# Performance work log

Hardware: AMD Instinct MI355X
Metric: run time of the kernel (lower is better)

## Reference

```python
import jax, jax.numpy as jnp
import numpy as np

NUM_NODES = 100000
NUM_EDGES = 1600000
FEAT = 128
HID = 128
NUM_GRAPHS = 512


def setup_inputs() -> dict:
    key = jax.random.key(0)
    ks = jax.random.split(key, 8)
    x = jax.random.normal(ks[0], (NUM_NODES, FEAT), dtype=jnp.float32)
    edge_index = jax.random.randint(ks[1], (2, NUM_EDGES), 0, NUM_NODES, dtype=jnp.int64)
    batch = jnp.sort(jax.random.randint(ks[2], (NUM_NODES,), 0, NUM_GRAPHS, dtype=jnp.int64))
    # Glorot-ish init for weights (scale named for clarity)
    s1 = 1.0 / np.sqrt(FEAT)
    s2 = 1.0 / np.sqrt(HID)
    W1 = jax.random.normal(ks[3], (FEAT, HID), dtype=jnp.float32) * s1
    b1 = jnp.zeros((HID,), dtype=jnp.float32)
    W2 = jax.random.normal(ks[4], (HID, HID), dtype=jnp.float32) * s2
    b2 = jnp.zeros((HID,), dtype=jnp.float32)
    Wout = jax.random.normal(ks[5], (HID, 1), dtype=jnp.float32) * s2
    bout = jnp.zeros((1,), dtype=jnp.float32)
    return {"x": x, "edge_index": edge_index, "batch": batch,
            "W1": W1, "b1": b1, "W2": W2, "b2": b2, "Wout": Wout, "bout": bout}


def reference(x, edge_index, batch, W1, b1, W2, b2, Wout, bout):
    N = x.shape[0]
    # PyG GCNConv: add self-loops, symmetric normalization D^-1/2 (A+I) D^-1/2
    loops = jnp.arange(N, dtype=edge_index.dtype)
    src = jnp.concatenate([edge_index[0], loops])  # [E+N]
    dst = jnp.concatenate([edge_index[1], loops])  # [E+N]
    ones = jnp.ones_like(dst, dtype=x.dtype)
    deg = jax.ops.segment_sum(ones, dst, num_segments=N)  # in-degree incl. self-loop
    dinv = jnp.where(deg > 0, jax.lax.rsqrt(deg), 0.0)
    coeff = (dinv[src] * dinv[dst])[:, None]  # [E+N, 1]

    def gcn(h, W, b):
        h = h @ W                                       # [N, H] dense GEMM
        msg = h[src] * coeff                            # gather + scale
        agg = jax.ops.segment_sum(msg, dst, num_segments=N)  # scatter-add
        return agg + b

    h = jax.nn.relu(gcn(x, W1, b1))
    h = jax.nn.relu(gcn(h, W2, b2))

    # global_mean_pool over batch ids
    G = NUM_GRAPHS
    sums = jax.ops.segment_sum(h, batch, num_segments=G)
    cnts = jax.ops.segment_sum(jnp.ones((N,), dtype=h.dtype), batch, num_segments=G)
    pooled = sums / jnp.maximum(cnts, 1.0)[:, None]

    return pooled @ Wout + bout  # [G, 1]
```

## Files before the change

kernel.cpp:

```cpp
#include <hip/hip_runtime.h>
#include <hip/hip_bf16.h>
#include <hip/hip_fp16.h>

#define FEAT 128
#define PSLOTS 64
#define BCAP 5120
#define NBIN 1024
#define NDEG 1024

typedef _Float16 h8 __attribute__((ext_vector_type(8)));
typedef float f4 __attribute__((ext_vector_type(4)));
typedef float fx2 __attribute__((ext_vector_type(2)));


__device__ __forceinline__ void wt_body(const float* __restrict__ W1,
                                        const float* __restrict__ W2,
                                        __half* __restrict__ Wt1,
                                        __half* __restrict__ Wt2, int bid) {
    int t = bid * 256 + threadIdx.x;
    const float* W = (t < 8192) ? W1 : W2;
    __half* Wt     = (t < 8192) ? Wt1 : Wt2;
    int u = t & 8191;
    int n = u >> 6, k2 = (u & 63) * 2;
    float a = W[(size_t)k2 * 128 + n];
    float b = W[(size_t)(k2 + 1) * 128 + n];
    ((__half2*)Wt)[n * 64 + (k2 >> 1)] = __floats2half2_rn(a, b);
}


__global__ __launch_bounds__(256) void k_pre(const int* __restrict__ ei, int E, int chunk,
                                             int* __restrict__ deg,
                                             const float* __restrict__ W1,
                                             const float* __restrict__ W2,
                                             __half* __restrict__ Wt1,
                                             __half* __restrict__ Wt2,
                                             unsigned char* __restrict__ padrow) {
    int bid = blockIdx.x;
    if (bid < NDEG) {
        int start = bid * chunk;
        int end = start + chunk; if (end > E) end = E;
        for (int e = start + threadIdx.x; e < end; e += 256)
            atomicAdd(&deg[ei[E + e]], 1);
    } else if (bid < NDEG + 64) {
        wt_body(W1, W2, Wt1, Wt2, bid - NDEG);
    } else {
        if (threadIdx.x < 8) ((uint4*)padrow)[threadIdx.x] = make_uint4(0, 0, 0, 0);
    }
}

__device__ __forceinline__ void bin_body(const int* __restrict__ ei, int E, int chunk,
                                         int* __restrict__ cursor,
                                         unsigned* __restrict__ binned, int nb,
                                         int bid, int* smem) {
    int* hist = smem;
    int* base = smem + 512;
    int start = bid * chunk;
    int end = start + chunk; if (end > E) end = E;
    for (int i = threadIdx.x; i < nb; i += 256) hist[i] = 0;
    __syncthreads();
    for (int e = start + threadIdx.x; e < end; e += 256)
        atomicAdd(&hist[ei[E + e] >> 8], 1);
    __syncthreads();
    for (int i = threadIdx.x; i < nb; i += 256) {
        int h = hist[i];
        base[i] = h ? atomicAdd(&cursor[i], h) : 0;
    }
    __syncthreads();
    for (int e = start + threadIdx.x; e < end; e += 256) {
        int s = ei[e];
        int d = ei[E + e];
        int b = d >> 8;
        int pos = atomicAdd(&base[b], 1);
        if (pos < BCAP)
            binned[(size_t)b * BCAP + pos] = (unsigned)s | ((unsigned)(d & 255) << 17);
    }
}


__device__ __forceinline__ void loadA(const __half* p, int quad, h8* a) {
#pragma unroll
    for (int ks = 0; ks < 4; ++ks)
        a[ks] = *(const h8*)(p + ks * 32 + quad * 8);
}
__device__ __forceinline__ void loadA(const float* p, int quad, h8* a) {
#pragma unroll
    for (int ks = 0; ks < 4; ++ks) {
        const float* q = p + ks * 32 + quad * 8;
        float4 f0 = *(const float4*)q;
        float4 f1 = *(const float4*)(q + 4);
        h8 v;
        v[0] = (_Float16)f0.x; v[1] = (_Float16)f0.y;
        v[2] = (_Float16)f0.z; v[3] = (_Float16)f0.w;
        v[4] = (_Float16)f1.x; v[5] = (_Float16)f1.y;
        v[6] = (_Float16)f1.z; v[7] = (_Float16)f1.w;
        a[ks] = v;
    }
}

template <typename TIN>
__device__ __forceinline__ void gemm_body(const TIN* __restrict__ X,
                                          const __half* __restrict__ Wt,
                                          unsigned char* __restrict__ Y, int N,
                                          const int* __restrict__ deg,
                                          int bid, _Float16* Bs) {
    {
        const float4* src = (const float4*)Wt;
        float4* dst = (float4*)Bs;
        for (int i = threadIdx.x; i < 2048; i += 256) {
            int n = i >> 4, ch = i & 15;
            dst[n * 16 + (ch ^ (n & 15))] = src[i];
        }
    }
    __syncthreads();

    int lane = threadIdx.x & 63;
    int wave = threadIdx.x >> 6;
    int m = lane & 15;
    int quad = lane >> 4;
    int rowb = bid * 128 + wave * 16;

    h8 a[2][4];
#pragma unroll
    for (int rt = 0; rt < 2; ++rt) {
        int rA = rowb + rt * 64 + m; if (rA >= N) rA = N - 1;
        loadA(X + (size_t)rA * FEAT, quad, a[rt]);
    }

    f4 acc[2][8];
#pragma unroll
    for (int rt = 0; rt < 2; ++rt)
#pragma unroll
        for (int nt = 0; nt < 8; ++nt) acc[rt][nt] = (f4){0.f, 0.f, 0.f, 0.f};

#pragma unroll
    for (int nt = 0; nt < 8; ++nt) {
        const _Float16* bbase = Bs + (nt * 16 + m) * 128;
#pragma unroll
        for (int ks = 0; ks < 4; ++ks) {
            int ch = (ks * 4 + quad) ^ m;
            h8 bfrag = *(const h8*)(bbase + ch * 8);
            acc[0][nt] = __builtin_amdgcn_mfma_f32_16x16x32_f16(a[0][ks], bfrag, acc[0][nt], 0, 0, 0);
            acc[1][nt] = __builtin_amdgcn_mfma_f32_16x16x32_f16(a[1][ks], bfrag, acc[1][nt], 0, 0, 0);
        }
    }

#pragma unroll
    for (int rt = 0; rt < 2; ++rt)
#pragma unroll
    for (int r = 0; r < 4; ++r) {
        int row = rowb + rt * 64 + quad * 4 + r;
        if (row < N) {
            float sc = rsqrtf((float)deg[row] + 1.0f);
#pragma unroll
            for (int nt = 0; nt < 8; ++nt) {
                float v = sc * acc[rt][nt][r];
                int pk = __builtin_amdgcn_cvt_pk_fp8_f32(v, v, 0, false);
                Y[(size_t)row * FEAT + nt * 16 + m] = (unsigned char)(pk & 0xFF);
            }
        }
    }
}


__global__ __launch_bounds__(256) void gemm_bin(const float* __restrict__ X,
                                                const __half* __restrict__ Wt1,
                                                unsigned char* __restrict__ Y,
                                                const int* __restrict__ deg,
                                                int N, int gemm_grid,
                                                const int* __restrict__ ei, int E, int chunk,
                                                int* __restrict__ cursor,
                                                unsigned* __restrict__ binned, int nb) {
    __shared__ __align__(16) char smem[32768];
    if ((int)blockIdx.x < gemm_grid)
        gemm_body<float>(X, Wt1, Y, N, deg, blockIdx.x, (_Float16*)smem);
    else
        bin_body(ei, E, chunk, cursor, binned, nb, blockIdx.x - gemm_grid, (int*)smem);
}


template <typename TIN>
__global__ __launch_bounds__(256) void gemm_mfma(const TIN* __restrict__ X,
                                                 const __half* __restrict__ Wt,
                                                 unsigned char* __restrict__ Y,
                                                 const int* __restrict__ deg, int N) {
    __shared__ __align__(16) _Float16 Bs[128 * 128];
    gemm_body<TIN>(X, Wt, Y, N, deg, blockIdx.x, Bs);
}


__global__ __launch_bounds__(256) void k_deg_fill(const unsigned* __restrict__ binned,
                                                  const int* __restrict__ cursor,
                                                  const int* __restrict__ deg,
                                                  int N, int* __restrict__ rowstart,
                                                  int* __restrict__ meta) {
    __shared__ int sc[256];
    __shared__ int cur[256];
    int b = blockIdx.x;
    int cnt = cursor[b]; if (cnt > BCAP) cnt = BCAP;
    int s = b * BCAP, e = s + cnt;
    int v = (b << 8) + threadIdx.x;
    int d = (v < N) ? deg[v] : 0;
    sc[threadIdx.x] = d;
    __syncthreads();
    for (int off = 1; off < 256; off <<= 1) {
        int t = (threadIdx.x >= off) ? sc[threadIdx.x - off] : 0;
        __syncthreads();
        sc[threadIdx.x] += t;
        __syncthreads();
    }
    int rs = s + sc[threadIdx.x] - d;
    cur[threadIdx.x] = rs;
    if (v < N) rowstart[v] = rs;
    __syncthreads();
    for (int i = s + threadIdx.x; i < e; i += 256) {
        unsigned p = binned[i];
        int src = (int)(p & 0x1FFFF);
        int drl = (int)(p >> 17);
        int pos = atomicAdd(&cur[drl], 1);
        meta[pos] = src << 7;
    }
    int zoff = N << 7;
    int t = cnt + threadIdx.x;
    if (threadIdx.x < 64 && t < BCAP) meta[s + t] = zoff;
}


__device__ __forceinline__ void accum8(uint2 u, float* acc) {
    fx2 p0 = __builtin_amdgcn_cvt_pk_f32_fp8((int)u.x, false);
    fx2 p1 = __builtin_amdgcn_cvt_pk_f32_fp8((int)u.x, true);
    fx2 p2 = __builtin_amdgcn_cvt_pk_f32_fp8((int)u.y, false);
    fx2 p3 = __builtin_amdgcn_cvt_pk_f32_fp8((int)u.y, true);
    acc[0] += p0.x; acc[1] += p0.y; acc[2] += p1.x; acc[3] += p1.y;
    acc[4] += p2.x; acc[5] += p2.y; acc[6] += p3.x; acc[7] += p3.y;
}

template <bool POOL>
__global__ __launch_bounds__(256) void agg_relu(const unsigned char* __restrict__ Y,
                                                const int* __restrict__ rowstart,
                                                const int* __restrict__ degc,
                                                const int* __restrict__ meta,
                                                const float* __restrict__ bias,
                                                __half* __restrict__ H, int N,
                                                const float* __restrict__ Wout,
                                                const int* __restrict__ batch,
                                                float* __restrict__ gsum, int G) {
    int wid  = (blockIdx.x * 256 + threadIdx.x) >> 6;
    int lane = threadIdx.x & 63;
    if (wid >= N) return;
    int v = wid;
    int g = lane >> 4;
    int c = lane & 15;
    int cb = c * 8;
    int zoff = N << 7;
    const char* Yb = (const char*)Y;

    float acc[8];
#pragma unroll
    for (int k = 0; k < 8; ++k) acc[k] = 0.f;

    {
        int so = (g == 0) ? (v << 7) : zoff;
        uint2 u = *(const uint2*)(Yb + so + cb);
        accum8(u, acc);
    }

    int base = rowstart[v];
    int n = degc[v];
    for (int i0 = 0; i0 < n; i0 += 32) {
        int o[8];
#pragma unroll
        for (int j = 0; j < 8; ++j) {
            int idx = i0 + g * 8 + j;
            int mj = meta[base + idx];
            o[j] = (idx < n) ? mj : zoff;
        }
        uint2 u[8];
#pragma unroll
        for (int j = 0; j < 8; ++j)
            u[j] = *(const uint2*)(Yb + o[j] + cb);
#pragma unroll
        for (int j = 0; j < 8; ++j) accum8(u[j], acc);
    }

#pragma unroll
    for (int k = 0; k < 8; ++k) {
        acc[k] += __shfl_xor(acc[k], 16);
        acc[k] += __shfl_xor(acc[k], 32);
    }
    float dv = rsqrtf((float)n + 1.0f);

    if (POOL) {
        const float4* bp = (const float4*)(bias + cb);
        float4 b0 = bp[0], b1 = bp[1];
        const float4* wp = (const float4*)(Wout + cb);
        float4 w0 = wp[0], w1 = wp[1];
        float h0 = fmaxf(dv * acc[0] + b0.x, 0.f);
        float h1 = fmaxf(dv * acc[1] + b0.y, 0.f);
        float h2 = fmaxf(dv * acc[2] + b0.z, 0.f);
        float h3 = fmaxf(dv * acc[3] + b0.w, 0.f);
        float h4 = fmaxf(dv * acc[4] + b1.x, 0.f);
        float h5 = fmaxf(dv * acc[5] + b1.y, 0.f);
        float h6 = fmaxf(dv * acc[6] + b1.z, 0.f);
        float h7 = fmaxf(dv * acc[7] + b1.w, 0.f);
        float s = h0 * w0.x + h1 * w0.y + h2 * w0.z + h3 * w0.w
                + h4 * w1.x + h5 * w1.y + h6 * w1.z + h7 * w1.w;
        if (g == 0) {
            s += __shfl_xor(s, 1);
            s += __shfl_xor(s, 2);
            s += __shfl_xor(s, 4);
            s += __shfl_xor(s, 8);
            if (lane == 0) {
                int slot = blockIdx.x & (PSLOTS - 1);
                atomicAdd(&gsum[slot * G + batch[v]], s);
            }
        }
    } else {
        float ax, ay;
        if (g == 0)      { ax = acc[0]; ay = acc[1]; }
        else if (g == 1) { ax = acc[2]; ay = acc[3]; }
        else if (g == 2) { ax = acc[4]; ay = acc[5]; }
        else             { ax = acc[6]; ay = acc[7]; }
        float2 bb = *(const float2*)(bias + cb + g * 2);
        float hx = fmaxf(dv * ax + bb.x, 0.f);
        float hy = fmaxf(dv * ay + bb.y, 0.f);
        *(__half2*)(H + (size_t)v * FEAT + cb + g * 2) = __floats2half2_rn(hx, hy);
    }
}


__global__ __launch_bounds__(256) void k_head(const float* __restrict__ gsum,
                                              const int* __restrict__ batch, int N, int G,
                                              const float* __restrict__ bout,
                                              float* __restrict__ out) {
    int g = blockIdx.x * 256 + threadIdx.x;
    if (g >= G) return;
    float s = 0.f;
#pragma unroll 8
    for (int k = 0; k < PSLOTS; ++k) s += gsum[k * G + g];
    int lo = 0, hi = N;
    while (lo < hi) { int mid = (lo + hi) >> 1; if (batch[mid] < g) lo = mid + 1; else hi = mid; }
    int start = lo;
    lo = start; hi = N;
    while (lo < hi) { int mid = (lo + hi) >> 1; if (batch[mid] < g + 1) lo = mid + 1; else hi = mid; }
    int cnt = lo - start;
    out[g] = s / (float)(cnt > 0 ? cnt : 1) + bout[0];
}


extern "C" void kernel_launch(void* const* d_in, const int* in_sizes, int n_in,
                              void* d_out, int out_size, void* d_ws, size_t ws_size,
                              hipStream_t stream) {
    const float* x    = (const float*)d_in[0];
    const int*   ei   = (const int*)d_in[1];
    const int*   batch= (const int*)d_in[2];
    const float* W1   = (const float*)d_in[3];
    const float* b1   = (const float*)d_in[4];
    const float* W2   = (const float*)d_in[5];
    const float* b2   = (const float*)d_in[6];
    const float* Wout = (const float*)d_in[7];
    const float* bout = (const float*)d_in[8];

    int N = in_sizes[0] / FEAT;
    int E = in_sizes[1] / 2;
    int G = out_size;
    int nb = (N + 255) >> 8;

    char* ws = (char*)d_ws;
    size_t off = 0;
    auto alloc = [&](size_t bytes) -> void* {
        void* p = ws + off;
        off += (bytes + 255) & ~(size_t)255;
        return p;
    };
    unsigned char* bufY = (unsigned char*)alloc((size_t)(N + 1) * FEAT);
    __half* bufH     = (__half*)alloc((size_t)N * FEAT * 2);
    __half* Wt1      = (__half*)alloc((size_t)FEAT * FEAT * 2);
    __half* Wt2      = (__half*)alloc((size_t)FEAT * FEAT * 2);
    size_t zbytes    = (size_t)PSLOTS * G * 4 + (size_t)nb * 4 + (size_t)N * 4;
    float* gsum      = (float*)alloc(zbytes);
    int*   cursor    = (int*)(gsum + (size_t)PSLOTS * G);
    int*   deg       = cursor + nb;
    int*   rowstart  = (int*)alloc((size_t)N * 4);
    unsigned* binned = (unsigned*)alloc((size_t)nb * BCAP * 4);
    int*   meta      = (int*)alloc((size_t)nb * BCAP * 4);

    int gemm_grid = (N + 127) / 128;
    int agg_grid  = (N + 3) / 4;
    int chunkD = (E + NDEG - 1) / NDEG;
    int chunkB = (E + NBIN - 1) / NBIN;

    hipMemsetAsync(gsum, 0, zbytes, stream);
    k_pre<<<NDEG + 65, 256, 0, stream>>>(ei, E, chunkD, deg, W1, W2, Wt1, Wt2,
                                         bufY + (size_t)N * FEAT);
    gemm_bin<<<gemm_grid + NBIN, 256, 0, stream>>>(x, Wt1, bufY, deg, N, gemm_grid,
                                                   ei, E, chunkB, cursor, binned, nb);
    k_deg_fill<<<nb, 256, 0, stream>>>(binned, cursor, deg, N, rowstart, meta);
    agg_relu<false><<<agg_grid, 256, 0, stream>>>(bufY, rowstart, deg, meta, b1, bufH, N,
                                                  nullptr, nullptr, nullptr, 0);
    gemm_mfma<__half><<<gemm_grid, 256, 0, stream>>>(bufH, Wt2, bufY, deg, N);
    agg_relu<true><<<agg_grid, 256, 0, stream>>>(bufY, rowstart, deg, meta, b2, nullptr, N,
                                                 Wout, batch, gsum, G);
    k_head<<<(G + 255) / 256, 256, 0, stream>>>(gsum, batch, N, G, bout, (float*)d_out);
}
```

Measured before the change: 342.1 us.

## Derive degrees from binned edges, dropping separate global-atomic degree pass

Removes the k_pre kernel that counted in-degrees with global atomics over all edges. Degrees are now counted in shared memory inside k_deg_fill from each bin's packed edges, and the weight transpose moves into a new bin_wt kernel, which uses half as many bin blocks. The first GEMM no longer overlaps with binning in a combined launch; it now runs as its own launch after k_deg_fill, because it needs the degrees. The zero pad row moves into the memset region and is addressed through a passed offset (zoff), and meta gains 64 extra padding entries.

```diff
diff --git a/kernel.cpp b/kernel.cpp
--- a/kernel.cpp
+++ b/kernel.cpp
@@ -5,8 +5,7 @@
 #define FEAT 128
 #define PSLOTS 64
 #define BCAP 5120
-#define NBIN 1024
-#define NDEG 1024
+#define NBIN 512
 
 typedef _Float16 h8 __attribute__((ext_vector_type(8)));
 typedef float f4 __attribute__((ext_vector_type(4)));
@@ -27,27 +26,6 @@
     ((__half2*)Wt)[n * 64 + (k2 >> 1)] = __floats2half2_rn(a, b);
 }
 
-
-__global__ __launch_bounds__(256) void k_pre(const int* __restrict__ ei, int E, int chunk,
-                                             int* __restrict__ deg,
-                                             const float* __restrict__ W1,
-                                             const float* __restrict__ W2,
-                                             __half* __restrict__ Wt1,
-                                             __half* __restrict__ Wt2,
-                                             unsigned char* __restrict__ padrow) {
-    int bid = blockIdx.x;
-    if (bid < NDEG) {
-        int start = bid * chunk;
-        int end = start + chunk; if (end > E) end = E;
-        for (int e = start + threadIdx.x; e < end; e += 256)
-            atomicAdd(&deg[ei[E + e]], 1);
-    } else if (bid < NDEG + 64) {
-        wt_body(W1, W2, Wt1, Wt2, bid - NDEG);
-    } else {
-        if (threadIdx.x < 8) ((uint4*)padrow)[threadIdx.x] = make_uint4(0, 0, 0, 0);
-    }
-}
-
 __device__ __forceinline__ void bin_body(const int* __restrict__ ei, int E, int chunk,
                                          int* __restrict__ cursor,
                                          unsigned* __restrict__ binned, int nb,
@@ -74,6 +52,20 @@
         if (pos < BCAP)
             binned[(size_t)b * BCAP + pos] = (unsigned)s | ((unsigned)(d & 255) << 17);
     }
+}
+
+__global__ __launch_bounds__(256) void bin_wt(const int* __restrict__ ei, int E, int chunk,
+                                              int* __restrict__ cursor,
+                                              unsigned* __restrict__ binned, int nb,
+                                              const float* __restrict__ W1,
+                                              const float* __restrict__ W2,
+                                              __half* __restrict__ Wt1,
+                                              __half* __restrict__ Wt2) {
+    __shared__ int smem[1024];
+    if ((int)blockIdx.x < NBIN)
+        bin_body(ei, E, chunk, cursor, binned, nb, blockIdx.x, smem);
+    else
+        wt_body(W1, W2, Wt1, Wt2, blockIdx.x - NBIN);
 }
 
 
@@ -161,23 +153,6 @@
     }
 }
 
-
-__global__ __launch_bounds__(256) void gemm_bin(const float* __restrict__ X,
-                                                const __half* __restrict__ Wt1,
-                                                unsigned char* __restrict__ Y,
-                                                const int* __restrict__ deg,
-                                                int N, int gemm_grid,
-                                                const int* __restrict__ ei, int E, int chunk,
-                                                int* __restrict__ cursor,
-                                                unsigned* __restrict__ binned, int nb) {
-    __shared__ __align__(16) char smem[32768];
-    if ((int)blockIdx.x < gemm_grid)
-        gemm_body<float>(X, Wt1, Y, N, deg, blockIdx.x, (_Float16*)smem);
-    else
-        bin_body(ei, E, chunk, cursor, binned, nb, blockIdx.x - gemm_grid, (int*)smem);
-}
-
-
 template <typename TIN>
 __global__ __launch_bounds__(256) void gemm_mfma(const TIN* __restrict__ X,
                                                  const __half* __restrict__ Wt,
@@ -190,16 +165,21 @@
 
 __global__ __launch_bounds__(256) void k_deg_fill(const unsigned* __restrict__ binned,
                                                   const int* __restrict__ cursor,
-                                                  const int* __restrict__ deg,
-                                                  int N, int* __restrict__ rowstart,
-                                                  int* __restrict__ meta) {
+                                                  int N, int* __restrict__ deg,
+                                                  int* __restrict__ rowstart,
+                                                  int* __restrict__ meta, int zoff) {
+    __shared__ int ld[256];
     __shared__ int sc[256];
     __shared__ int cur[256];
     int b = blockIdx.x;
     int cnt = cursor[b]; if (cnt > BCAP) cnt = BCAP;
     int s = b * BCAP, e = s + cnt;
-    int v = (b << 8) + threadIdx.x;
-    int d = (v < N) ? deg[v] : 0;
+    ld[threadIdx.x] = 0;
+    __syncthreads();
+    for (int i = s + threadIdx.x; i < e; i += 256)
+        atomicAdd(&ld[binned[i] >> 17], 1);
+    __syncthreads();
+    int d = ld[threadIdx.x];
     sc[threadIdx.x] = d;
     __syncthreads();
     for (int off = 1; off < 256; off <<= 1) {
@@ -210,7 +190,11 @@
     }
     int rs = s + sc[threadIdx.x] - d;
     cur[threadIdx.x] = rs;
-    if (v < N) rowstart[v] = rs;
+    int v = (b << 8) + threadIdx.x;
+    if (v < N) {
+        deg[v] = d;
+        rowstart[v] = rs;
+    }
     __syncthreads();
     for (int i = s + threadIdx.x; i < e; i += 256) {
         unsigned p = binned[i];
@@ -219,9 +203,8 @@
         int pos = atomicAdd(&cur[drl], 1);
         meta[pos] = src << 7;
     }
-    int zoff = N << 7;
     int t = cnt + threadIdx.x;
-    if (threadIdx.x < 64 && t < BCAP) meta[s + t] = zoff;
+    if (threadIdx.x < 64 && t < BCAP + 64) meta[s + t] = zoff;
 }
 
 
@@ -240,7 +223,7 @@
                                                 const int* __restrict__ degc,
                                                 const int* __restrict__ meta,
                                                 const float* __restrict__ bias,
-                                                __half* __restrict__ H, int N,
+                                                __half* __restrict__ H, int N, int zoff,
                                                 const float* __restrict__ Wout,
                                                 const int* __restrict__ batch,
                                                 float* __restrict__ gsum, int G) {
@@ -251,7 +234,6 @@
     int g = lane >> 4;
     int c = lane & 15;
     int cb = c * 8;
-    int zoff = N << 7;
     const char* Yb = (const char*)Y;
 
     float acc[8];
@@ -372,33 +354,34 @@
         off += (bytes + 255) & ~(size_t)255;
         return p;
     };
-    unsigned char* bufY = (unsigned char*)alloc((size_t)(N + 1) * FEAT);
+    unsigned char* bufY = (unsigned char*)alloc((size_t)N * FEAT);
     __half* bufH     = (__half*)alloc((size_t)N * FEAT * 2);
     __half* Wt1      = (__half*)alloc((size_t)FEAT * FEAT * 2);
     __half* Wt2      = (__half*)alloc((size_t)FEAT * FEAT * 2);
-    size_t zbytes    = (size_t)PSLOTS * G * 4 + (size_t)nb * 4 + (size_t)N * 4;
-    float* gsum      = (float*)alloc(zbytes);
+    size_t zbytes    = 256 + (size_t)PSLOTS * G * 4 + (size_t)nb * 4 + (size_t)N * 4;
+    char*  zr        = (char*)alloc(zbytes);
+    unsigned char* padrow = (unsigned char*)zr;
+    float* gsum      = (float*)(zr + 256);
     int*   cursor    = (int*)(gsum + (size_t)PSLOTS * G);
     int*   deg       = cursor + nb;
+    int    zoff      = (int)((char*)padrow - (char*)bufY);
     int*   rowstart  = (int*)alloc((size_t)N * 4);
     unsigned* binned = (unsigned*)alloc((size_t)nb * BCAP * 4);
-    int*   meta      = (int*)alloc((size_t)nb * BCAP * 4);
+    int*   meta      = (int*)alloc(((size_t)nb * BCAP + 64) * 4);
 
     int gemm_grid = (N + 127) / 128;
     int agg_grid  = (N + 3) / 4;
-    int chunkD = (E + NDEG - 1) / NDEG;
     int chunkB = (E + NBIN - 1) / NBIN;
 
-    hipMemsetAsync(gsum, 0, zbytes, stream);
-    k_pre<<<NDEG + 65, 256, 0, stream>>>(ei, E, chunkD, deg, W1, W2, Wt1, Wt2,
-                                         bufY + (size_t)N * FEAT);
-    gemm_bin<<<gemm_grid + NBIN, 256, 0, stream>>>(x, Wt1, bufY, deg, N, gemm_grid,
-                                                   ei, E, chunkB, cursor, binned, nb);
-    k_deg_fill<<<nb, 256, 0, stream>>>(binned, cursor, deg, N, rowstart, meta);
-    agg_relu<false><<<agg_grid, 256, 0, stream>>>(bufY, rowstart, deg, meta, b1, bufH, N,
+    hipMemsetAsync(zr, 0, zbytes, stream);
+    bin_wt<<<NBIN + 64, 256, 0, stream>>>(ei, E, chunkB, cursor, binned, nb,
+                                          W1, W2, Wt1, Wt2);
+    k_deg_fill<<<nb, 256, 0, stream>>>(binned, cursor, N, deg, rowstart, meta, zoff);
+    gemm_mfma<float><<<gemm_grid, 256, 0, stream>>>(x, Wt1, bufY, deg, N);
+    agg_relu<false><<<agg_grid, 256, 0, stream>>>(bufY, rowstart, deg, meta, b1, bufH, N, zoff,
                                                   nullptr, nullptr, nullptr, 0);
     gemm_mfma<__half><<<gemm_grid, 256, 0, stream>>>(bufH, Wt2, bufY, deg, N);
-    agg_relu<true><<<agg_grid, 256, 0, stream>>>(bufY, rowstart, deg, meta, b2, nullptr, N,
+    agg_relu<true><<<agg_grid, 256, 0, stream>>>(bufY, rowstart, deg, meta, b2, nullptr, N, zoff,
                                                  Wout, batch, gsum, G);
     k_head<<<(G + 255) / 256, 256, 0, stream>>>(gsum, batch, N, G, bout, (float*)d_out);
 }
```

Result: faster. 285.9 us (-16.4%).
